# Performance work log

Measured on AMD Instinct MI355X. Metric: run time of the kernel, lower is better.

Reference implementation:

```python
import jax, jax.numpy as jnp
import numpy as np

EPS = 1e-5

def _layernorm(x, g, b):
    # LayerNorm over last dim (head_dim), eps=1e-5 like nn.LayerNorm
    mu = jnp.mean(x, axis=-1, keepdims=True)
    var = jnp.mean(jnp.square(x - mu), axis=-1, keepdims=True)
    return (x - mu) * jax.lax.rsqrt(var + EPS) * g + b

def _rotate_half(x):
    d = x.shape[-1] // 2
    return jnp.concatenate([-x[..., d:], x[..., :d]], axis=-1)

def _apply_rotary(x, cos, sin):
    # x: [B,S,H,D]; cos/sin: [S,D] broadcast over batch and heads
    c = cos[None, :, None, :]
    s = sin[None, :, None, :]
    return x * c + _rotate_half(x) * s

def setup_inputs() -> dict:
    key = jax.random.key(0)
    ks = jax.random.split(key, 16)
    B, S, Dm = 2, 1024, 2048
    H, Hkv, Dh = 16, 4, 128
    f = lambda k, shp: (jax.random.normal(k, shp, dtype=jnp.float32) * 0.02)
    return {
        "hidden_states": jax.random.normal(ks[0], (B, S, Dm), dtype=jnp.float32),
        "cos": jax.random.uniform(ks[1], (S, Dh), dtype=jnp.float32),
        "sin": jax.random.uniform(ks[2], (S, Dh), dtype=jnp.float32),
        "Wq": f(ks[3], (H * Dh, Dm)),   "bq": jnp.zeros((H * Dh,), jnp.float32),
        "Wk": f(ks[4], (Hkv * Dh, Dm)), "bk": jnp.zeros((Hkv * Dh,), jnp.float32),
        "Wv": f(ks[5], (Hkv * Dh, Dm)), "bv": jnp.zeros((Hkv * Dh,), jnp.float32),
        "Wo": f(ks[6], (Dm, H * Dh)),   "bo": jnp.zeros((Dm,), jnp.float32),
        "qn_g": jnp.ones((Dh,), jnp.float32), "qn_b": jnp.zeros((Dh,), jnp.float32),
        "kn_g": jnp.ones((Dh,), jnp.float32), "kn_b": jnp.zeros((Dh,), jnp.float32),
        "cu_seqlens": jnp.array([0, S, 2 * S], dtype=jnp.int32),
        "max_s": 1024,
    }

def reference(hidden_states, cos, sin, Wq, bq, Wk, bk, Wv, bv, Wo, bo,
              qn_g, qn_b, kn_g, kn_b, cu_seqlens, max_s):
    B, S, Dm = hidden_states.shape
    Dh = qn_g.shape[0]
    H = Wq.shape[0] // Dh
    Hkv = Wk.shape[0] // Dh
    scale = 1.0 / jnp.sqrt(jnp.float32(Dh))

    q = (hidden_states @ Wq.T + bq).reshape(B, S, H, Dh)
    k = (hidden_states @ Wk.T + bk).reshape(B, S, Hkv, Dh)
    v = (hidden_states @ Wv.T + bv).reshape(B, S, Hkv, Dh)

    q = _apply_rotary(_layernorm(q, qn_g, qn_b), cos, sin)
    k = _apply_rotary(_layernorm(k, kn_g, kn_b), cos, sin)

    # GQA: repeat_interleave kv heads to match q heads
    n_rep = H // Hkv
    if n_rep > 1:
        k = jnp.repeat(k, n_rep, axis=2)
        v = jnp.repeat(v, n_rep, axis=2)

    # scores: [B,H,S,S]
    scores = jnp.einsum('bqhd,bkhd->bhqk', q, k) * scale
    causal = jnp.tril(jnp.ones((S, S), dtype=bool))
    scores = jnp.where(causal[None, None], scores, jnp.finfo(scores.dtype).min)
    weights = jax.nn.softmax(scores, axis=-1)
    out = jnp.einsum('bhqk,bkhd->bqhd', weights, v).reshape(B, S, H * Dh)
    return out @ Wo.T + bo
```

## Files before the change

kernel.cpp:

```cpp
#include <hip/hip_runtime.h>
#include <cmath>

typedef __attribute__((ext_vector_type(8))) short bf16x8;
typedef __attribute__((ext_vector_type(4))) short s16x4;
typedef __attribute__((ext_vector_type(4))) float f32x4;

#define MFMA_BF16 __builtin_amdgcn_mfma_f32_16x16x32_bf16

__device__ __forceinline__ float bf2f(short s) {
    unsigned u = ((unsigned)(unsigned short)s) << 16;
    return __builtin_bit_cast(float, u);
}
__device__ __forceinline__ short f2bf(float f) {
    unsigned u = __builtin_bit_cast(unsigned, f);
    u += 0x7fffu + ((u >> 16) & 1u);
    return (short)(u >> 16);
}

__device__ __forceinline__ void gl_lds16(const short* gp, short* lp) {
    __builtin_amdgcn_global_load_lds(
        (const __attribute__((address_space(1))) unsigned int*)gp,
        (__attribute__((address_space(3))) unsigned int*)lp, 16, 0, 0);
}

__global__ __launch_bounds__(256) void cvt5(
    const float* s0, short* d0, int n0,
    const float* s1, short* d1, int n1,
    const float* s2, short* d2, int n2,
    const float* s3, short* d3, int n3,
    const float* s4, short* d4, int n4)
{
    long long i = (long long)blockIdx.x * 1024 + threadIdx.x * 4;
    const float* s; short* d;
    if      (i < n0)                  { s = s0; d = d0; }
    else if ((i -= n0) < n1)          { s = s1; d = d1; }
    else if ((i -= n1) < n2)          { s = s2; d = d2; }
    else if ((i -= n2) < n3)          { s = s3; d = d3; }
    else      { i -= n3;                s = s4; d = d4; }
    float4 v = *(const float4*)(s + i);
    s16x4 o;
    o[0] = f2bf(v.x); o[1] = f2bf(v.y); o[2] = f2bf(v.z); o[3] = f2bf(v.w);
    *(s16x4*)(d + i) = o;
}

template <int MODE>
__global__ __launch_bounds__(256) void gemm_t(
    const short* __restrict__ A, const short* __restrict__ W,
    const float* __restrict__ bq, const float* __restrict__ bk,
    const float* __restrict__ bv,
    short* __restrict__ qo, short* __restrict__ ko, short* __restrict__ vo,
    float* __restrict__ fo,
    int M, int K, int S, int Hkv, int Nq, int Nkv, int N)
{
    __shared__ __align__(16) short As[2][2 * 8 * 512];
    __shared__ __align__(16) short Bs[2][2 * 4 * 512];

    const int w    = threadIdx.x >> 6;
    const int lane = threadIdx.x & 63;
    const int l15  = lane & 15;
    const int quad = lane >> 4;
    const int wy   = w >> 1;
    const int wx   = w & 1;

    unsigned gx = gridDim.x, gy = gridDim.y;
    unsigned bx = blockIdx.x, by = blockIdx.y;
    if ((gx & 3) == 0 && (gy & 1) == 0) {
        unsigned lin = by * gx + bx;
        unsigned xcd = lin & 7, idx = lin >> 3;
        unsigned n   = gx >> 2;
        bx = (xcd & 3) * n + idx % n;
        by = (xcd >> 2) * (gy >> 1) + idx / n;
    }
    const int m0 = by * 128;
    const int n0 = bx * 64;

    const short* Ab = A + (size_t)m0 * K;
    const short* Wb = W + (size_t)n0 * K;

    const int srow = lane >> 2;
    const int scol = ((lane & 3) ^ ((srow >> 1) & 3)) * 8;
    auto stage = [&](int buf, int kofs) {
#pragma unroll
        for (int h2 = 0; h2 < 2; h2++) {
#pragma unroll
            for (int i = 0; i < 2; i++) {
                const int c = 2 * w + i;
                gl_lds16(Ab + (size_t)(c * 16 + srow) * K + kofs + h2 * 32 + scol,
                         As[buf] + h2 * 4096 + c * 512 + lane * 8);
            }
            gl_lds16(Wb + (size_t)(w * 16 + srow) * K + kofs + h2 * 32 + scol,
                     Bs[buf] + h2 * 2048 + w * 512 + lane * 8);
        }
    };

    f32x4 acc[4][2];
#pragma unroll
    for (int i = 0; i < 4; i++)
#pragma unroll
        for (int j = 0; j < 2; j++) acc[i][j] = f32x4{0.f, 0.f, 0.f, 0.f};

    const int ridx = (l15 * 4 + (quad ^ ((l15 >> 1) & 3))) * 8;
    const int nk = K / 64;
    stage(0, 0);
    __syncthreads();

    for (int kt = 0; kt < nk; kt++) {
        const int cur = kt & 1;
        if (kt + 1 < nk) stage(cur ^ 1, (kt + 1) * 64);

#pragma unroll
        for (int h2 = 0; h2 < 2; h2++) {
            bf16x8 af[4], bfr[2];
#pragma unroll
            for (int i = 0; i < 4; i++)
                af[i] = *(const bf16x8*)(As[cur] + h2 * 4096 + (wy * 4 + i) * 512 + ridx);
#pragma unroll
            for (int j = 0; j < 2; j++)
                bfr[j] = *(const bf16x8*)(Bs[cur] + h2 * 2048 + (wx * 2 + j) * 512 + ridx);
#pragma unroll
            for (int i = 0; i < 4; i++)
#pragma unroll
                for (int j = 0; j < 2; j++)
                    acc[i][j] = MFMA_BF16(af[i], bfr[j], acc[i][j], 0, 0, 0);
        }
        __syncthreads();
    }

#pragma unroll
    for (int i = 0; i < 4; i++) {
#pragma unroll
        for (int j = 0; j < 2; j++) {
            const int col = n0 + wx * 32 + j * 16 + l15;
#pragma unroll
            for (int r = 0; r < 4; r++) {
                const int row = m0 + wy * 64 + i * 16 + quad * 4 + r;
                float v = acc[i][j][r];
                if constexpr (MODE == 0) {
                    if (col < Nq) {
                        qo[(size_t)row * Nq + col] = f2bf(v + bq[col]);
                    } else if (col < Nq + Nkv) {
                        int cn = col - Nq;
                        ko[(size_t)row * Nkv + cn] = f2bf(v + bk[cn]);
                    } else {
                        int cn = col - Nq - Nkv;
                        int b  = row / S, s = row - b * S;
                        int hk = cn >> 7, dh = cn & 127;
                        vo[(size_t)((b * Hkv + hk) * 128 + dh) * S + s] = f2bf(v + bv[cn]);
                    }
                } else {
                    fo[(size_t)row * N + col] = v + bq[col];
                }
            }
        }
    }
}

__global__ __launch_bounds__(256) void ln_rope2(
    const short* __restrict__ Xq, short* __restrict__ Yq,
    const short* __restrict__ Xk, short* __restrict__ Yk,
    const float* __restrict__ qg, const float* __restrict__ qbe,
    const float* __restrict__ kg, const float* __restrict__ kbe,
    const float* __restrict__ cosp, const float* __restrict__ sinp,
    int H, int Hkv, int S, int nq)
{
    int gw = blockIdx.x * 4 + (threadIdx.x >> 6);
    const int lane = threadIdx.x & 63;
    const short* X; short* Y; const float* g; const float* bt; int Hc;
    if (gw < nq) { X = Xq; Y = Yq; g = qg; bt = qbe; Hc = H; }
    else { gw -= nq; X = Xk; Y = Yk; g = kg; bt = kbe; Hc = Hkv; }

    const int h  = gw % Hc;
    const int rs = gw / Hc;
    const int b  = rs / S;
    const int s  = rs - b * S;

    const short* x = X + ((size_t)rs * Hc + h) * 128;
    float x0 = bf2f(x[lane]), x1 = bf2f(x[lane + 64]);

    float sum = x0 + x1;
    float sq  = x0 * x0 + x1 * x1;
#pragma unroll
    for (int off = 32; off > 0; off >>= 1) {
        sum += __shfl_xor(sum, off, 64);
        sq  += __shfl_xor(sq, off, 64);
    }
    float mu  = sum * (1.f / 128.f);
    float var = sq * (1.f / 128.f) - mu * mu;
    float rinv = rsqrtf(var + 1e-5f);

    float y0 = (x0 - mu) * rinv * g[lane]      + bt[lane];
    float y1 = (x1 - mu) * rinv * g[lane + 64] + bt[lane + 64];

    float c0 = cosp[(size_t)s * 128 + lane];
    float c1 = cosp[(size_t)s * 128 + lane + 64];
    float s0 = sinp[(size_t)s * 128 + lane];
    float s1 = sinp[(size_t)s * 128 + lane + 64];

    float o0 = y0 * c0 - y1 * s0;
    float o1 = y1 * c1 + y0 * s1;

    short* yp = Y + ((size_t)(b * Hc + h) * S + s) * 128;
    yp[lane]      = f2bf(o0);
    yp[lane + 64] = f2bf(o1);
}

__global__ __launch_bounds__(256, 2) void attn(
    const short* __restrict__ Q, const short* __restrict__ Kt,
    const short* __restrict__ Vt, short* __restrict__ O,
    int S, int H, int Hkv, int nrep, float scale)
{
    __shared__ __align__(16) short Ks[2][16 * 512];
    __shared__ __align__(16) short Vs[2][16 * 512];
    __shared__ __align__(16) short P[4][16][72];

    const int w    = threadIdx.x >> 6;
    const int lane = threadIdx.x & 63;
    const int l15  = lane & 15;
    const int quad = lane >> 4;
    const int bh   = blockIdx.x;
    const int h    = bh % H;
    const int b    = bh / H;
    const int nyt  = gridDim.y;
    const int y    = blockIdx.y;
    const int qblk = (y < (nyt >> 1)) ? (nyt - 1 - y) : (y - (nyt >> 1));
    const int hk   = h / nrep;
    const int m0   = qblk * 64 + w * 16;
    const int qpos = m0 + l15;

    const short* qb = Q  + (size_t)(b * H + h) * S * 128;
    const short* kb = Kt + (size_t)(b * Hkv + hk) * S * 128;
    const short* vb = Vt + (size_t)(b * Hkv + hk) * 128 * S;

    auto stage = [&](int buf, int j0) {
#pragma unroll
        for (int i = 0; i < 8; i++) {
            if (w < 2) {
                const int s = w * 8 + i;
                const int t = s >> 2, c = s & 3;
                gl_lds16(kb + (size_t)(j0 + t * 16 + l15) * 128 + c * 32 + quad * 8,
                         Ks[buf] + s * 512 + lane * 8);
            } else {
                const int u = (w - 2) * 8 + i;
                const int c = u >> 1, hf = u & 1;
                gl_lds16(vb + (size_t)(c * 16 + l15) * S + j0 + hf * 32 + quad * 8,
                         Vs[buf] + u * 512 + lane * 8);
            }
        }
    };

    bf16x8 qf[4];
#pragma unroll
    for (int c = 0; c < 4; c++)
        qf[c] = *(const bf16x8*)(qb + (size_t)(m0 + l15) * 128 + c * 32 + quad * 8);

    f32x4 of[8];
#pragma unroll
    for (int c = 0; c < 8; c++) of[c] = f32x4{0.f, 0.f, 0.f, 0.f};
    float m_s = -1e30f, l_s = 0.f;
    const float c2 = scale * 1.44269504f;

    const int nkt = qblk + 1;
    stage(0, 0);
    __syncthreads();

    for (int kt = 0; kt < nkt; kt++) {
        const int cur = kt & 1;
        if (kt + 1 < nkt) stage(cur ^ 1, (kt + 1) * 64);

        const short* Kb = Ks[cur];
        const short* Vb = Vs[cur];
        const int j0 = kt * 64;

        f32x4 sc[4];
#pragma unroll
        for (int t = 0; t < 4; t++) sc[t] = f32x4{0.f, 0.f, 0.f, 0.f};
        __builtin_amdgcn_s_setprio(1);
#pragma unroll
        for (int c = 0; c < 4; c++)
#pragma unroll
            for (int t = 0; t < 4; t++) {
                bf16x8 kf = *(const bf16x8*)(Kb + (t * 4 + c) * 512 + lane * 8);
                sc[t] = MFMA_BF16(kf, qf[c], sc[t], 0, 0, 0);
            }
        __builtin_amdgcn_s_setprio(0);

        float v[4][4];
        float mx = -1e30f;
#pragma unroll
        for (int t = 0; t < 4; t++)
#pragma unroll
            for (int r = 0; r < 4; r++) {
                float s_ = sc[t][r];
                if (j0 + t * 16 + quad * 4 + r > qpos) s_ = -1e30f;
                v[t][r] = s_;
                mx = fmaxf(mx, s_);
            }
        mx = fmaxf(mx, __shfl_xor(mx, 16, 64));
        mx = fmaxf(mx, __shfl_xor(mx, 32, 64));

        if (!__all((mx - m_s) * c2 <= 8.f)) {
            float mnew  = fmaxf(m_s, mx);
            float alpha = exp2f((m_s - mnew) * c2);
            l_s *= alpha;
#pragma unroll
            for (int c = 0; c < 8; c++) {
                f32x4 t = of[c];
                t[0] *= alpha; t[1] *= alpha; t[2] *= alpha; t[3] *= alpha;
                of[c] = t;
            }
            m_s = mnew;
        }
        const float mc = m_s * c2;

        float sum = 0.f;
        float p[4][4];
#pragma unroll
        for (int t = 0; t < 4; t++)
#pragma unroll
            for (int r = 0; r < 4; r++) {
                p[t][r] = exp2f(__builtin_fmaf(v[t][r], c2, -mc));
                sum += p[t][r];
            }
        sum += __shfl_xor(sum, 16, 64);
        sum += __shfl_xor(sum, 32, 64);
        l_s += sum;

#pragma unroll
        for (int t = 0; t < 4; t++) {
            s16x4 pk;
#pragma unroll
            for (int r = 0; r < 4; r++) pk[r] = f2bf(p[t][r]);
            *(s16x4*)(&P[w][l15][t * 16 + quad * 4]) = pk;
        }
        bf16x8 pb0 = *(const bf16x8*)(&P[w][l15][quad * 8]);
        bf16x8 pb1 = *(const bf16x8*)(&P[w][l15][32 + quad * 8]);

        __builtin_amdgcn_s_setprio(1);
#pragma unroll
        for (int c = 0; c < 8; c++) {
            bf16x8 vf0 = *(const bf16x8*)(Vb + (c * 2 + 0) * 512 + lane * 8);
            bf16x8 vf1 = *(const bf16x8*)(Vb + (c * 2 + 1) * 512 + lane * 8);
            of[c] = MFMA_BF16(vf0, pb0, of[c], 0, 0, 0);
            of[c] = MFMA_BF16(vf1, pb1, of[c], 0, 0, 0);
        }
        __builtin_amdgcn_s_setprio(0);
        __syncthreads();
    }

    const int HDh = H * 128;
    const float rinv = 1.0f / l_s;
    short* orow = O + ((size_t)b * S + qpos) * HDh + h * 128;
#pragma unroll
    for (int c = 0; c < 8; c++) {
        s16x4 ov;
#pragma unroll
        for (int r = 0; r < 4; r++) ov[r] = f2bf(of[c][r] * rinv);
        *(s16x4*)(orow + c * 16 + quad * 4) = ov;
    }
}

extern "C" void kernel_launch(void* const* d_in, const int* in_sizes, int n_in,
                              void* d_out, int out_size, void* d_ws, size_t ws_size,
                              hipStream_t stream) {
    const float* hs   = (const float*)d_in[0];
    const float* cosp = (const float*)d_in[1];
    const float* sinp = (const float*)d_in[2];
    const float* Wq   = (const float*)d_in[3];
    const float* bq   = (const float*)d_in[4];
    const float* Wk   = (const float*)d_in[5];
    const float* bk   = (const float*)d_in[6];
    const float* Wv   = (const float*)d_in[7];
    const float* bv   = (const float*)d_in[8];
    const float* Wo   = (const float*)d_in[9];
    const float* bo   = (const float*)d_in[10];
    const float* qg   = (const float*)d_in[11];
    const float* qb_  = (const float*)d_in[12];
    const float* kg   = (const float*)d_in[13];
    const float* kb_  = (const float*)d_in[14];

    const int Dh    = in_sizes[11];
    const int Dm    = in_sizes[10];
    const int HDh   = in_sizes[4];
    const int H     = HDh / Dh;
    const int HkvDh = in_sizes[6];
    const int Hkv   = HkvDh / Dh;
    const int S     = in_sizes[1] / Dh;
    const int B     = in_sizes[0] / (S * Dm);
    const int M     = B * S;
    const int nrep  = H / Hkv;

    char* ws = (char*)d_ws;
    short* hsb  = (short*)ws;  ws += (size_t)M * Dm      * 2;
    short* Wqb  = (short*)ws;  ws += (size_t)HDh * Dm    * 2;
    short* Wkb  = (short*)ws;  ws += (size_t)HkvDh * Dm  * 2;
    short* Wvb  = (short*)ws;  ws += (size_t)HkvDh * Dm  * 2;
    short* Wob  = (short*)ws;  ws += (size_t)Dm * HDh    * 2;
    short* qg16 = (short*)ws;  ws += (size_t)M * HDh     * 2;
    short* kg16 = (short*)ws;  ws += (size_t)M * HkvDh   * 2;
    short* qbuf = (short*)ws;  ws += (size_t)M * HDh     * 2;
    short* kbuf = (short*)ws;  ws += (size_t)M * HkvDh   * 2;
    short* vbuf = (short*)ws;  ws += (size_t)M * HkvDh   * 2;
    short* abuf = qg16;

    dim3 blk(256);
    const int n0 = M * Dm, n1 = HDh * Dm, n2 = HkvDh * Dm, n3 = HkvDh * Dm, n4 = Dm * HDh;
    cvt5<<<dim3((n0 + n1 + n2 + n3 + n4) / 1024), blk, 0, stream>>>(
        hs, hsb, n0, Wq, Wqb, n1, Wk, Wkb, n2, Wv, Wvb, n3, Wo, Wob, n4);

    const int Ntot = HDh + 2 * HkvDh;
    gemm_t<0><<<dim3(Ntot / 64, M / 128), blk, 0, stream>>>(
        hsb, Wqb, bq, bk, bv, qg16, kg16, vbuf, nullptr,
        M, Dm, S, Hkv, HDh, HkvDh, Ntot);

    const int nq = M * H;
    ln_rope2<<<dim3((nq + M * Hkv) / 4), blk, 0, stream>>>(
        qg16, qbuf, kg16, kbuf, qg, qb_, kg, kb_, cosp, sinp, H, Hkv, S, nq);

    const float scale = 1.0f / sqrtf((float)Dh);
    attn<<<dim3(H * B, S / 64), blk, 0, stream>>>(qbuf, kbuf, vbuf, abuf, S, H, Hkv, nrep, scale);

    gemm_t<1><<<dim3(Dm / 64, M / 128), blk, 0, stream>>>(
        abuf, Wob, bo, nullptr, nullptr, nullptr, nullptr, nullptr, (float*)d_out,
        M, HDh, S, Hkv, Dm, 0, Dm);
}
```

Before: 246.1 us.

## Fuse Q layernorm and rotary into attention prologue, drop lazy rescale and setprio

Moves the query LayerNorm and RoPE out of the separate ln_rope2 pass and into the attention kernel's Q-fragment load. Q is now read straight from the projection output in [B,S,H*Dh] layout, normalized with a one-pass sum/sum-of-squares, rotated and packed into bf16 MFMA operands. This removes a full write and read of the Q intermediate, at the cost of extra prologue work per attention block. It also replaces the conditional lazy-rescale softmax with unconditional per-tile rescaling and removes the s_setprio hints around the MFMA loops.

```diff
diff --git a/kernel.cpp b/kernel.cpp
--- a/kernel.cpp
+++ b/kernel.cpp
@@ -205,8 +205,10 @@
 }
 
 __global__ __launch_bounds__(256, 2) void attn(
-    const short* __restrict__ Q, const short* __restrict__ Kt,
+    const short* __restrict__ Qr, const short* __restrict__ Kt,
     const short* __restrict__ Vt, short* __restrict__ O,
+    const float* __restrict__ qga, const float* __restrict__ qbe,
+    const float* __restrict__ cosp, const float* __restrict__ sinp,
     int S, int H, int Hkv, int nrep, float scale)
 {
     __shared__ __align__(16) short Ks[2][16 * 512];
@@ -227,7 +229,6 @@
     const int m0   = qblk * 64 + w * 16;
     const int qpos = m0 + l15;
 
-    const short* qb = Q  + (size_t)(b * H + h) * S * 128;
     const short* kb = Kt + (size_t)(b * Hkv + hk) * S * 128;
     const short* vb = Vt + (size_t)(b * Hkv + hk) * 128 * S;
 
@@ -248,10 +249,56 @@
         }
     };
 
+    const int HDh = H * 128;
+    const short* qraw = Qr + (size_t)(b * S + qpos) * HDh + h * 128 + quad * 8;
+    float yv[4][8];
+    float sum = 0.f, sq = 0.f;
+#pragma unroll
+    for (int c = 0; c < 4; c++) {
+        bf16x8 qv = *(const bf16x8*)(qraw + c * 32);
+#pragma unroll
+        for (int e = 0; e < 8; e++) {
+            float x = bf2f(qv[e]);
+            yv[c][e] = x; sum += x; sq += x * x;
+        }
+    }
+    sum += __shfl_xor(sum, 16, 64); sum += __shfl_xor(sum, 32, 64);
+    sq  += __shfl_xor(sq , 16, 64); sq  += __shfl_xor(sq , 32, 64);
+    {
+        float mu  = sum * (1.f / 128.f);
+        float var = sq * (1.f / 128.f) - mu * mu;
+        float rin = rsqrtf(var + 1e-5f);
+#pragma unroll
+        for (int c = 0; c < 4; c++) {
+            const int d0 = c * 32 + quad * 8;
+            float4 g0 = *(const float4*)(qga + d0);
+            float4 g1 = *(const float4*)(qga + d0 + 4);
+            float4 b0 = *(const float4*)(qbe + d0);
+            float4 b1 = *(const float4*)(qbe + d0 + 4);
+            float gg[8] = {g0.x,g0.y,g0.z,g0.w,g1.x,g1.y,g1.z,g1.w};
+            float bb[8] = {b0.x,b0.y,b0.z,b0.w,b1.x,b1.y,b1.z,b1.w};
+#pragma unroll
+            for (int e = 0; e < 8; e++)
+                yv[c][e] = (yv[c][e] - mu) * rin * gg[e] + bb[e];
+        }
+    }
     bf16x8 qf[4];
 #pragma unroll
-    for (int c = 0; c < 4; c++)
-        qf[c] = *(const bf16x8*)(qb + (size_t)(m0 + l15) * 128 + c * 32 + quad * 8);
+    for (int c = 0; c < 4; c++) {
+        const int d0 = c * 32 + quad * 8;
+        const float* cp = cosp + (size_t)qpos * 128 + d0;
+        const float* sp = sinp + (size_t)qpos * 128 + d0;
+        float4 c0v = *(const float4*)cp, c1v = *(const float4*)(cp + 4);
+        float4 s0v = *(const float4*)sp, s1v = *(const float4*)(sp + 4);
+        float cc[8] = {c0v.x,c0v.y,c0v.z,c0v.w,c1v.x,c1v.y,c1v.z,c1v.w};
+        float ss[8] = {s0v.x,s0v.y,s0v.z,s0v.w,s1v.x,s1v.y,s1v.z,s1v.w};
+        const float sgn = (c < 2) ? -1.f : 1.f;
+#pragma unroll
+        for (int e = 0; e < 8; e++) {
+            float o = yv[c][e] * cc[e] + sgn * yv[c ^ 2][e] * ss[e];
+            qf[c][e] = f2bf(o);
+        }
+    }
 
     f32x4 of[8];
 #pragma unroll
@@ -274,7 +321,6 @@
         f32x4 sc[4];
 #pragma unroll
         for (int t = 0; t < 4; t++) sc[t] = f32x4{0.f, 0.f, 0.f, 0.f};
-        __builtin_amdgcn_s_setprio(1);
 #pragma unroll
         for (int c = 0; c < 4; c++)
 #pragma unroll
@@ -282,7 +328,6 @@
                 bf16x8 kf = *(const bf16x8*)(Kb + (t * 4 + c) * 512 + lane * 8);
                 sc[t] = MFMA_BF16(kf, qf[c], sc[t], 0, 0, 0);
             }
-        __builtin_amdgcn_s_setprio(0);
 
         float v[4][4];
         float mx = -1e30f;
@@ -297,33 +342,29 @@
             }
         mx = fmaxf(mx, __shfl_xor(mx, 16, 64));
         mx = fmaxf(mx, __shfl_xor(mx, 32, 64));
-
-        if (!__all((mx - m_s) * c2 <= 8.f)) {
-            float mnew  = fmaxf(m_s, mx);
-            float alpha = exp2f((m_s - mnew) * c2);
-            l_s *= alpha;
-#pragma unroll
-            for (int c = 0; c < 8; c++) {
-                f32x4 t = of[c];
-                t[0] *= alpha; t[1] *= alpha; t[2] *= alpha; t[3] *= alpha;
-                of[c] = t;
-            }
-            m_s = mnew;
-        }
-        const float mc = m_s * c2;
-
-        float sum = 0.f;
+        float mnew  = fmaxf(m_s, mx);
+        float mc    = mnew * c2;
+        float alpha = exp2f(m_s * c2 - mc);
+        float sum2 = 0.f;
         float p[4][4];
 #pragma unroll
         for (int t = 0; t < 4; t++)
 #pragma unroll
             for (int r = 0; r < 4; r++) {
                 p[t][r] = exp2f(__builtin_fmaf(v[t][r], c2, -mc));
-                sum += p[t][r];
-            }
-        sum += __shfl_xor(sum, 16, 64);
-        sum += __shfl_xor(sum, 32, 64);
-        l_s += sum;
+                sum2 += p[t][r];
+            }
+        sum2 += __shfl_xor(sum2, 16, 64);
+        sum2 += __shfl_xor(sum2, 32, 64);
+        l_s = l_s * alpha + sum2;
+        m_s = mnew;
+
+#pragma unroll
+        for (int c = 0; c < 8; c++) {
+            f32x4 t = of[c];
+            t[0] *= alpha; t[1] *= alpha; t[2] *= alpha; t[3] *= alpha;
+            of[c] = t;
+        }
 
 #pragma unroll
         for (int t = 0; t < 4; t++) {
@@ -335,7 +376,6 @@
         bf16x8 pb0 = *(const bf16x8*)(&P[w][l15][quad * 8]);
         bf16x8 pb1 = *(const bf16x8*)(&P[w][l15][32 + quad * 8]);
 
-        __builtin_amdgcn_s_setprio(1);
 #pragma unroll
         for (int c = 0; c < 8; c++) {
             bf16x8 vf0 = *(const bf16x8*)(Vb + (c * 2 + 0) * 512 + lane * 8);
@@ -343,11 +383,9 @@
             of[c] = MFMA_BF16(vf0, pb0, of[c], 0, 0, 0);
             of[c] = MFMA_BF16(vf1, pb1, of[c], 0, 0, 0);
         }
-        __builtin_amdgcn_s_setprio(0);
         __syncthreads();
     }
 
-    const int HDh = H * 128;
     const float rinv = 1.0f / l_s;
     short* orow = O + ((size_t)b * S + qpos) * HDh + h * 128;
 #pragma unroll
@@ -397,10 +435,9 @@
     short* Wob  = (short*)ws;  ws += (size_t)Dm * HDh    * 2;
     short* qg16 = (short*)ws;  ws += (size_t)M * HDh     * 2;
     short* kg16 = (short*)ws;  ws += (size_t)M * HkvDh   * 2;
-    short* qbuf = (short*)ws;  ws += (size_t)M * HDh     * 2;
+    short* abuf = (short*)ws;  ws += (size_t)M * HDh     * 2;
     short* kbuf = (short*)ws;  ws += (size_t)M * HkvDh   * 2;
     short* vbuf = (short*)ws;  ws += (size_t)M * HkvDh   * 2;
-    short* abuf = qg16;
 
     dim3 blk(256);
     const int n0 = M * Dm, n1 = HDh * Dm, n2 = HkvDh * Dm, n3 = HkvDh * Dm, n4 = Dm * HDh;
@@ -412,12 +449,12 @@
         hsb, Wqb, bq, bk, bv, qg16, kg16, vbuf, nullptr,
         M, Dm, S, Hkv, HDh, HkvDh, Ntot);
 
-    const int nq = M * H;
-    ln_rope2<<<dim3((nq + M * Hkv) / 4), blk, 0, stream>>>(
-        qg16, qbuf, kg16, kbuf, qg, qb_, kg, kb_, cosp, sinp, H, Hkv, S, nq);
+    ln_rope2<<<dim3((M * Hkv) / 4), blk, 0, stream>>>(
+        kg16, kbuf, kg16, kbuf, kg, kb_, kg, kb_, cosp, sinp, Hkv, Hkv, S, 0);
 
     const float scale = 1.0f / sqrtf((float)Dh);
-    attn<<<dim3(H * B, S / 64), blk, 0, stream>>>(qbuf, kbuf, vbuf, abuf, S, H, Hkv, nrep, scale);
+    attn<<<dim3(H * B, S / 64), blk, 0, stream>>>(
+        qg16, kbuf, vbuf, abuf, qg, qb_, cosp, sinp, S, H, Hkv, nrep, scale);
 
     gemm_t<1><<<dim3(Dm / 64, M / 128), blk, 0, stream>>>(
         abuf, Wob, bo, nullptr, nullptr, nullptr, nullptr, nullptr, (float*)d_out,
```

Result: faster. 235.9 us (median of 2 runs) (-4.1%).
